# Optimization experiments

Measured on AMD Instinct MI355X. Metric: run time of the kernel, lower is better.

## Reference

```python
import jax, jax.numpy as jnp
import numpy as np

N_NODES = 50000
N_EDGES = 600000
D = 128
EPS = 1e-5
AVG_D_LOG = float(np.log(4 + 1))  # avg_d={'log': log(avg_d+1)}, avg_d=4


def setup_inputs() -> dict:
    key = jax.random.key(0)
    ks = jax.random.split(key, 8)
    h = jax.random.normal(ks[0], (N_NODES, D), dtype=jnp.float32)
    # guarantee every node has at least one incoming edge (self-loop)
    edge_dst = jnp.concatenate([
        jnp.arange(N_NODES, dtype=jnp.int64),
        jax.random.randint(ks[1], (N_EDGES - N_NODES,), 0, N_NODES).astype(jnp.int64),
    ])
    edge_src = jax.random.randint(ks[2], (N_EDGES,), 0, N_NODES).astype(jnp.int64)
    def lin(k, fan_in, fan_out):
        lim = 1.0 / np.sqrt(fan_in)
        return jax.random.uniform(k, (fan_in, fan_out), jnp.float32, -lim, lim)
    W_pre = lin(ks[3], 2 * D, D)
    b_pre = jnp.zeros((D,), jnp.float32)
    W_post = lin(ks[4], 12 * D + D, D)  # 4 aggregators * 3 scalers * D + in_dim
    b_post = jnp.zeros((D,), jnp.float32)
    W_mix = lin(ks[5], D, D)
    b_mix = jnp.zeros((D,), jnp.float32)
    return {"h": h, "edge_src": edge_src, "edge_dst": edge_dst,
            "W_pre": W_pre, "b_pre": b_pre, "W_post": W_post,
            "b_post": b_post, "W_mix": W_mix, "b_mix": b_mix}


def reference(h, edge_src, edge_dst, W_pre, b_pre, W_post, b_post, W_mix, b_mix):
    n = h.shape[0]
    # pretrans_edges: cat(src, dst) -> Linear -> ReLU (MLP act) -> ReLU (outer)
    z2 = jnp.concatenate([h[edge_src], h[edge_dst]], axis=1)        # [E, 2D]
    e = jax.nn.relu(z2 @ W_pre + b_pre)                             # [E, D]
    # multi-aggregator segment reduce over destination nodes
    deg = jax.ops.segment_sum(jnp.ones_like(edge_dst, jnp.float32), edge_dst, n)  # [N]
    inv_deg = 1.0 / deg[:, None]
    mean = jax.ops.segment_sum(e, edge_dst, n) * inv_deg
    mean_sq = jax.ops.segment_sum(e * e, edge_dst, n) * inv_deg
    std = jnp.sqrt(jax.nn.relu(mean_sq - mean * mean) + EPS)
    mx = jax.ops.segment_max(e, edge_dst, n)
    mn = jax.ops.segment_min(e, edge_dst, n)
    agg = jnp.concatenate([mean, mx, mn, std], axis=1)              # [N, 4D]
    # scalers: identity, amplification, attenuation
    log_d = jnp.log(deg + 1.0)[:, None]
    scaled = jnp.concatenate([agg, agg * (log_d / AVG_D_LOG), agg * (AVG_D_LOG / log_d)], axis=1)  # [N, 12D]
    # posttrans: cat(h, aggregated) -> Linear -> ReLU
    hp = jax.nn.relu(jnp.concatenate([h, scaled], axis=1) @ W_post + b_post)  # [N, D]
    # mixing network + residual (node_dim == out_dim)
    out = h + jax.nn.leaky_relu(hp @ W_mix + b_mix, negative_slope=0.01)
    return out
```

## Files before the change

### kernel.cpp

```cpp
#include <hip/hip_runtime.h>
#include <hip/hip_bf16.h>

#define N_NODES 50000
#define N_EDGES 600000
#define D 128
#define NB_SCAN 196

constexpr float AVG_D_LOG = 1.6094379124341003f;
constexpr float EPS_V = 1e-5f;

#define PQ_B     0ul
#define AGG_B    25600000ul
#define HBF_B    76800000ul
#define WPRET2_B 89600000ul
#define WPOSTT_B 89665536ul
#define WMIXT_B  90091520ul
#define DEGC_B   90124288ul
#define OFF_B    90324288ul
#define CUR_B    90524352ul
#define SRCS_B   90724352ul
#define BSUM_B   93124352ul

typedef __attribute__((ext_vector_type(8))) short bf16x8;
typedef __attribute__((ext_vector_type(4))) float f32x4;

__device__ __forceinline__ short f2b(float f) {
    unsigned u = __builtin_bit_cast(unsigned, f);
    u += 0x7fffu + ((u >> 16) & 1u);
    return (short)(u >> 16);
}
__device__ __forceinline__ unsigned pk2(float a, float b) {
    return (unsigned)(unsigned short)f2b(a) | ((unsigned)(unsigned short)f2b(b) << 16);
}
__device__ __forceinline__ float blo(unsigned u) { return __uint_as_float(u << 16); }
__device__ __forceinline__ float bhi(unsigned u) { return __uint_as_float(u & 0xffff0000u); }

__global__ __launch_bounds__(256) void prep_kernel(
    const float* __restrict__ h, const float* __restrict__ Wpre,
    const float* __restrict__ Wpost, const float* __restrict__ Wmix,
    short* __restrict__ hbf, short* __restrict__ wpreT2,
    short* __restrict__ wpostT, short* __restrict__ wmixT,
    int* __restrict__ degc, int* __restrict__ cursor)
{
    long i = (long)blockIdx.x * 256 + threadIdx.x;
    if (i < 6400000) { hbf[i] = f2b(h[i]); return; }
    i -= 6400000;
    if (i < 32768) {
        int n = i >> 7, k = i & 127;
        float v = (n < 128) ? Wpre[k * 128 + n] : Wpre[(k + 128) * 128 + (n - 128)];
        wpreT2[n * 128 + k] = f2b(v);
        return;
    }
    i -= 32768;
    if (i < 212992) { int k = i >> 7, n = i & 127; wpostT[n * 1664 + k] = f2b(Wpost[k * 128 + n]); return; }
    i -= 212992;
    if (i < 16384) { int k = i >> 7, n = i & 127; wmixT[n * 128 + k] = f2b(Wmix[k * 128 + n]); return; }
    i -= 16384;
    if (i < N_NODES) { degc[i] = 0; return; }
    i -= N_NODES;
    if (i < N_NODES) cursor[i] = 0;
}

__global__ __launch_bounds__(256) void hist_kernel(const int* __restrict__ edst, int* __restrict__ degc) {
    int e = blockIdx.x * 256 + threadIdx.x;
    if (e < N_EDGES) atomicAdd(&degc[edst[e]], 1);
}

__global__ __launch_bounds__(256) void scan1_kernel(const int* __restrict__ degc, int* __restrict__ bsum) {
    int n = blockIdx.x * 256 + threadIdx.x;
    int v = (n < N_NODES) ? degc[n] : 0;
#pragma unroll
    for (int o = 32; o > 0; o >>= 1) v += __shfl_down(v, o);
    __shared__ int w4[4];
    if ((threadIdx.x & 63) == 0) w4[threadIdx.x >> 6] = v;
    __syncthreads();
    if (threadIdx.x == 0) bsum[blockIdx.x] = w4[0] + w4[1] + w4[2] + w4[3];
}

__global__ void scan2_kernel(int* __restrict__ bsum, int* __restrict__ off) {
    if (threadIdx.x == 0 && blockIdx.x == 0) {
        int r = 0;
        for (int i = 0; i < NB_SCAN; i++) { int t = bsum[i]; bsum[i] = r; r += t; }
        off[N_NODES] = r;
    }
}

__global__ __launch_bounds__(256) void scan3_kernel(const int* __restrict__ degc,
                                                    const int* __restrict__ bsum, int* __restrict__ off) {
    __shared__ int sd[256];
    int tid = threadIdx.x;
    int n = blockIdx.x * 256 + tid;
    int v = (n < N_NODES) ? degc[n] : 0;
    sd[tid] = v;
    __syncthreads();
    for (int o = 1; o < 256; o <<= 1) {
        int t = (tid >= o) ? sd[tid - o] : 0;
        __syncthreads();
        sd[tid] += t;
        __syncthreads();
    }
    if (n < N_NODES) off[n] = sd[tid] - v + bsum[blockIdx.x];
}

__global__ __launch_bounds__(256) void scatter_kernel(const int* __restrict__ esrc, const int* __restrict__ edst,
                                                      const int* __restrict__ off, int* __restrict__ cursor,
                                                      int* __restrict__ srcs) {
    int e = blockIdx.x * 256 + threadIdx.x;
    if (e < N_EDGES) {
        int d = edst[e];
        int p = off[d] + atomicAdd(&cursor[d], 1);
        srcs[p] = esrc[e];
    }
}

__global__ __launch_bounds__(256) void gemm_pq_kernel(
    const short* __restrict__ hbf, const short* __restrict__ wpreT2,
    const float* __restrict__ bpre, short* __restrict__ PQ)
{
    __shared__ __align__(16) short As[128][72];
    __shared__ __align__(16) short Bs[256][72];

    const int tid = threadIdx.x;
    const int bn = blockIdx.x * 128;
    const int lane = tid & 63, wv = tid >> 6;
    const int lm = lane & 15, quad = lane >> 4;

    f32x4 acc[2][16];
#pragma unroll
    for (int a = 0; a < 2; a++)
#pragma unroll
        for (int b = 0; b < 16; b++) acc[a][b] = (f32x4){0.f, 0.f, 0.f, 0.f};

#pragma unroll
    for (int kc = 0; kc < 2; kc++) {
        __syncthreads();
#pragma unroll
        for (int t = 0; t < 4; t++) {
            int q = tid + t * 256;
            int m = q >> 3, seg = q & 7;
            int n = bn + m; if (n >= N_NODES) n = N_NODES - 1;
            *(int4*)&As[m][seg * 8] = *(const int4*)(hbf + (long)n * 128 + kc * 64 + seg * 8);
        }
#pragma unroll
        for (int t = 0; t < 8; t++) {
            int q = tid + t * 256;
            int n = q >> 3, seg = q & 7;
            *(int4*)&Bs[n][seg * 8] = *(const int4*)(wpreT2 + n * 128 + kc * 64 + seg * 8);
        }
        __syncthreads();
#pragma unroll
        for (int ks = 0; ks < 2; ks++) {
            const int ko = ks * 32 + quad * 8;
            bf16x8 a0 = *(const bf16x8*)&As[wv * 32 + lm][ko];
            bf16x8 a1 = *(const bf16x8*)&As[wv * 32 + 16 + lm][ko];
#pragma unroll
            for (int ct = 0; ct < 16; ct++) {
                bf16x8 b = *(const bf16x8*)&Bs[ct * 16 + lm][ko];
                acc[0][ct] = __builtin_amdgcn_mfma_f32_16x16x32_bf16(b, a0, acc[0][ct], 0, 0, 0);
                acc[1][ct] = __builtin_amdgcn_mfma_f32_16x16x32_bf16(b, a1, acc[1][ct], 0, 0, 0);
            }
        }
    }

#pragma unroll
    for (int rt = 0; rt < 2; rt++) {
        int row = wv * 32 + rt * 16 + lm;
        int n = bn + row;
        if (n >= N_NODES) continue;
        short* dst = PQ + (long)n * 256;
#pragma unroll
        for (int ct = 0; ct < 16; ct++) {
            int col = ct * 16 + quad * 4;
            float v0 = acc[rt][ct][0], v1 = acc[rt][ct][1], v2 = acc[rt][ct][2], v3 = acc[rt][ct][3];
            if (ct >= 8) {
                float4 bv = *(const float4*)(bpre + (col - 128));
                v0 += bv.x; v1 += bv.y; v2 += bv.z; v3 += bv.w;
            }
            int2 pkd; pkd.x = (int)pk2(v0, v1); pkd.y = (int)pk2(v2, v3);
            *(int2*)(dst + col) = pkd;
        }
    }
}

__global__ __launch_bounds__(256) void edgestats_kernel(
    const short* __restrict__ PQ, const int* __restrict__ srcs,
    const int* __restrict__ off, short* __restrict__ aggbf)
{
    const int wv = threadIdx.x >> 6, lane = threadIdx.x & 63;
    const int n = blockIdx.x * 4 + wv;
    const unsigned* Pb = (const unsigned*)PQ;

    const int s0 = __builtin_amdgcn_readfirstlane(off[n]);
    const int s1 = __builtin_amdgcn_readfirstlane(off[n + 1]);

    unsigned qu = Pb[(long)n * 128 + 64 + lane];
    const float qa = blo(qu), qb = bhi(qu);

    float sA = 0.f, sB = 0.f, qA = 0.f, qB = 0.f;
    float mxA = -1e30f, mxB = -1e30f, mnA = 1e30f, mnB = 1e30f;

    int p = s0;
    for (; p + 4 <= s1; p += 4) {
        int i0 = srcs[p], i1 = srcs[p + 1], i2 = srcs[p + 2], i3 = srcs[p + 3];
        unsigned u0 = Pb[(long)i0 * 128 + lane];
        unsigned u1 = Pb[(long)i1 * 128 + lane];
        unsigned u2 = Pb[(long)i2 * 128 + lane];
        unsigned u3 = Pb[(long)i3 * 128 + lane];
#pragma unroll
        for (int j = 0; j < 4; j++) {
            unsigned u = (j == 0) ? u0 : (j == 1) ? u1 : (j == 2) ? u2 : u3;
            float a = blo(u) + qa; a = a > 0.f ? a : 0.f;
            float b = bhi(u) + qb; b = b > 0.f ? b : 0.f;
            sA += a; sB += b; qA += a * a; qB += b * b;
            mxA = fmaxf(mxA, a); mxB = fmaxf(mxB, b);
            mnA = fminf(mnA, a); mnB = fminf(mnB, b);
        }
    }
    for (; p < s1; p++) {
        unsigned u = Pb[(long)srcs[p] * 128 + lane];
        float a = blo(u) + qa; a = a > 0.f ? a : 0.f;
        float b = bhi(u) + qb; b = b > 0.f ? b : 0.f;
        sA += a; sB += b; qA += a * a; qB += b * b;
        mxA = fmaxf(mxA, a); mxB = fmaxf(mxB, b);
        mnA = fminf(mnA, a); mnB = fminf(mnB, b);
    }

    float inv = 1.0f / (float)(s1 - s0);
    float mA = sA * inv, mB = sB * inv;
    float vA = qA * inv - mA * mA; vA = vA > 0.f ? vA : 0.f;
    float vB = qB * inv - mB * mB; vB = vB > 0.f ? vB : 0.f;
    float stA = sqrtf(vA + EPS_V), stB = sqrtf(vB + EPS_V);

    unsigned* ag = (unsigned*)(aggbf + (long)n * 512);
    ag[lane]       = pk2(mA, mB);
    ag[64 + lane]  = pk2(mxA, mxB);
    ag[128 + lane] = pk2(mnA, mnB);
    ag[192 + lane] = pk2(stA, stB);
}

__global__ __launch_bounds__(256) void node_kernel(
    const float* __restrict__ h, const short* __restrict__ hbf, const short* __restrict__ aggbf,
    const int* __restrict__ degc, const short* __restrict__ wpostT, const float* __restrict__ bpost,
    const short* __restrict__ wmixT, const float* __restrict__ bmix, float* __restrict__ out)
{
    __shared__ __align__(16) short As[128][72];
    __shared__ __align__(16) short Bs[128][72];
    __shared__ float sAmp[128], sAtt[128];

    const int tid = threadIdx.x;
    const int bn = blockIdx.x * 128;
    if (tid < 128) {
        int n = bn + tid; if (n >= N_NODES) n = N_NODES - 1;
        float d = (float)degc[n];
        float ld = logf(d + 1.0f);
        sAmp[tid] = ld * (1.0f / AVG_D_LOG);
        sAtt[tid] = AVG_D_LOG / ld;
    }
    __syncthreads();

    const int lane = tid & 63, wv = tid >> 6;
    const int lm = lane & 15, quad = lane >> 4;

    f32x4 acc[2][8];
#pragma unroll
    for (int a = 0; a < 2; a++)
#pragma unroll
        for (int b = 0; b < 8; b++) acc[a][b] = (f32x4){0.f, 0.f, 0.f, 0.f};

    for (int c = 0; c < 26; c++) {
        __syncthreads();
        const int r = c >> 1;
        const int half = (c & 1) * 64;
#pragma unroll
        for (int t = 0; t < 4; t++) {
            int q = tid + t * 256;
            int m = q >> 3, seg = q & 7;
            int n = bn + m; if (n >= N_NODES) n = N_NODES - 1;
            int4 v;
            if (r == 0) {
                v = *(const int4*)(hbf + (long)n * 128 + half + seg * 8);
            } else {
                int a = (r - 1) & 3, s = (r - 1) >> 2;
                v = *(const int4*)(aggbf + (long)n * 512 + a * 128 + half + seg * 8);
                if (s) {
                    float sc = (s == 1) ? sAmp[m] : sAtt[m];
                    unsigned* pu = (unsigned*)&v;
#pragma unroll
                    for (int j = 0; j < 4; j++) {
                        unsigned u = pu[j];
                        pu[j] = pk2(blo(u) * sc, bhi(u) * sc);
                    }
                }
            }
            *(int4*)&As[m][seg * 8] = v;
        }
#pragma unroll
        for (int t = 0; t < 4; t++) {
            int q = tid + t * 256;
            int n = q >> 3, seg = q & 7;
            *(int4*)&Bs[n][seg * 8] = *(const int4*)(wpostT + n * 1664 + c * 64 + seg * 8);
        }
        __syncthreads();
#pragma unroll
        for (int ks = 0; ks < 2; ks++) {
            const int ko = ks * 32 + quad * 8;
            bf16x8 a0 = *(const bf16x8*)&As[wv * 32 + lm][ko];
            bf16x8 a1 = *(const bf16x8*)&As[wv * 32 + 16 + lm][ko];
#pragma unroll
            for (int ct = 0; ct < 8; ct++) {
                bf16x8 b = *(const bf16x8*)&Bs[ct * 16 + lm][ko];
                acc[0][ct] = __builtin_amdgcn_mfma_f32_16x16x32_bf16(b, a0, acc[0][ct], 0, 0, 0);
                acc[1][ct] = __builtin_amdgcn_mfma_f32_16x16x32_bf16(b, a1, acc[1][ct], 0, 0, 0);
            }
        }
    }

#pragma unroll
    for (int rt = 0; rt < 2; rt++)
#pragma unroll
        for (int ct = 0; ct < 8; ct++) {
            float4 bv = *(const float4*)(bpost + ct * 16 + quad * 4);
            float v0 = acc[rt][ct][0] + bv.x; acc[rt][ct][0] = v0 > 0.f ? v0 : 0.f;
            float v1 = acc[rt][ct][1] + bv.y; acc[rt][ct][1] = v1 > 0.f ? v1 : 0.f;
            float v2 = acc[rt][ct][2] + bv.z; acc[rt][ct][2] = v2 > 0.f ? v2 : 0.f;
            float v3 = acc[rt][ct][3] + bv.w; acc[rt][ct][3] = v3 > 0.f ? v3 : 0.f;
        }

    f32x4 acc2[2][8];
#pragma unroll
    for (int a = 0; a < 2; a++)
#pragma unroll
        for (int b = 0; b < 8; b++) acc2[a][b] = (f32x4){0.f, 0.f, 0.f, 0.f};

#pragma unroll
    for (int kc = 0; kc < 2; kc++) {
        __syncthreads();
#pragma unroll
        for (int ctl = 0; ctl < 4; ctl++) {
            int ct = kc * 4 + ctl;
#pragma unroll
            for (int rt = 0; rt < 2; rt++) {
                int row = wv * 32 + rt * 16 + lm;
                int col = ctl * 16 + quad * 4;
                int2 pkd;
                pkd.x = (int)pk2(acc[rt][ct][0], acc[rt][ct][1]);
                pkd.y = (int)pk2(acc[rt][ct][2], acc[rt][ct][3]);
                *(int2*)&As[row][col] = pkd;
            }
        }
#pragma unroll
        for (int t = 0; t < 4; t++) {
            int q = tid + t * 256;
            int n = q >> 3, seg = q & 7;
            *(int4*)&Bs[n][seg * 8] = *(const int4*)(wmixT + n * 128 + kc * 64 + seg * 8);
        }
        __syncthreads();
#pragma unroll
        for (int ks = 0; ks < 2; ks++) {
            const int ko = ks * 32 + quad * 8;
            bf16x8 a0 = *(const bf16x8*)&As[wv * 32 + lm][ko];
            bf16x8 a1 = *(const bf16x8*)&As[wv * 32 + 16 + lm][ko];
#pragma unroll
            for (int ct = 0; ct < 8; ct++) {
                bf16x8 b = *(const bf16x8*)&Bs[ct * 16 + lm][ko];
                acc2[0][ct] = __builtin_amdgcn_mfma_f32_16x16x32_bf16(b, a0, acc2[0][ct], 0, 0, 0);
                acc2[1][ct] = __builtin_amdgcn_mfma_f32_16x16x32_bf16(b, a1, acc2[1][ct], 0, 0, 0);
            }
        }
    }

#pragma unroll
    for (int rt = 0; rt < 2; rt++) {
        int row = wv * 32 + rt * 16 + lm;
        int n = bn + row;
        if (n >= N_NODES) continue;
#pragma unroll
        for (int ct = 0; ct < 8; ct++) {
            int col = ct * 16 + quad * 4;
            float4 bv = *(const float4*)(bmix + col);
            float4 hv = *(const float4*)(h + (long)n * 128 + col);
            float4 o;
            float v0 = acc2[rt][ct][0] + bv.x; v0 = v0 > 0.f ? v0 : 0.01f * v0; o.x = hv.x + v0;
            float v1 = acc2[rt][ct][1] + bv.y; v1 = v1 > 0.f ? v1 : 0.01f * v1; o.y = hv.y + v1;
            float v2 = acc2[rt][ct][2] + bv.z; v2 = v2 > 0.f ? v2 : 0.01f * v2; o.z = hv.z + v2;
            float v3 = acc2[rt][ct][3] + bv.w; v3 = v3 > 0.f ? v3 : 0.01f * v3; o.w = hv.w + v3;
            *(float4*)(out + (long)n * 128 + col) = o;
        }
    }
}

extern "C" void kernel_launch(void* const* d_in, const int* in_sizes, int n_in,
                              void* d_out, int out_size, void* d_ws, size_t ws_size,
                              hipStream_t stream) {
    const float* h     = (const float*)d_in[0];
    const int*   esrc  = (const int*)d_in[1];
    const int*   edst  = (const int*)d_in[2];
    const float* Wpre  = (const float*)d_in[3];
    const float* bpre  = (const float*)d_in[4];
    const float* Wpost = (const float*)d_in[5];
    const float* bpost = (const float*)d_in[6];
    const float* Wmix  = (const float*)d_in[7];
    const float* bmix  = (const float*)d_in[8];
    float* out = (float*)d_out;
    char* ws = (char*)d_ws;

    short* PQ     = (short*)(ws + PQ_B);
    short* aggbf  = (short*)(ws + AGG_B);
    short* hbf    = (short*)(ws + HBF_B);
    short* wpreT2 = (short*)(ws + WPRET2_B);
    short* wpostT = (short*)(ws + WPOSTT_B);
    short* wmixT  = (short*)(ws + WMIXT_B);
    int*   degc   = (int*)(ws + DEGC_B);
    int*   off    = (int*)(ws + OFF_B);
    int*   cursor = (int*)(ws + CUR_B);
    int*   srcs   = (int*)(ws + SRCS_B);
    int*   bsum   = (int*)(ws + BSUM_B);

    prep_kernel<<<26415, 256, 0, stream>>>(h, Wpre, Wpost, Wmix, hbf, wpreT2, wpostT, wmixT, degc, cursor);
    hist_kernel<<<(N_EDGES + 255) / 256, 256, 0, stream>>>(edst, degc);
    scan1_kernel<<<NB_SCAN, 256, 0, stream>>>(degc, bsum);
    scan2_kernel<<<1, 64, 0, stream>>>(bsum, off);
    scan3_kernel<<<NB_SCAN, 256, 0, stream>>>(degc, bsum, off);
    scatter_kernel<<<(N_EDGES + 255) / 256, 256, 0, stream>>>(esrc, edst, off, cursor, srcs);
    gemm_pq_kernel<<<(N_NODES + 127) / 128, 256, 0, stream>>>(hbf, wpreT2, bpre, PQ);
    edgestats_kernel<<<N_NODES / 4, 256, 0, stream>>>(PQ, srcs, off, aggbf);
    node_kernel<<<(N_NODES + 127) / 128, 256, 0, stream>>>(h, hbf, aggbf, degc, wpostT, bpost, wmixT, bmix, out);
}
```

Measured before the change: 295.0 us.

## Factor degree scalers out of post GEMM into three accumulators; parallelize block scan

The node kernel no longer builds the amplified and attenuated aggregate copies in shared memory. The same aggregate tile is multiplied by three weight slices into separate accumulators, which are combined per row with amp and att scalars after the K loop. This drops the per-element bf16 rescaling and cuts K iterations from 26 to 10, with the node tile halved to 64 rows to fit the three accumulator sets. The single-thread block-sum scan is also replaced by a 256-thread shared-memory scan. The cost is a larger Bs tile, more registers per thread, and twice as many blocks, each reloading the full weight matrix.

```diff
diff --git a/kernel.cpp b/kernel.cpp
--- a/kernel.cpp
+++ b/kernel.cpp
@@ -77,12 +77,20 @@
     if (threadIdx.x == 0) bsum[blockIdx.x] = w4[0] + w4[1] + w4[2] + w4[3];
 }
 
-__global__ void scan2_kernel(int* __restrict__ bsum, int* __restrict__ off) {
-    if (threadIdx.x == 0 && blockIdx.x == 0) {
-        int r = 0;
-        for (int i = 0; i < NB_SCAN; i++) { int t = bsum[i]; bsum[i] = r; r += t; }
-        off[N_NODES] = r;
-    }
+__global__ __launch_bounds__(256) void scan2_kernel(int* __restrict__ bsum, int* __restrict__ off) {
+    __shared__ int sd[256];
+    int tid = threadIdx.x;
+    int v = (tid < NB_SCAN) ? bsum[tid] : 0;
+    sd[tid] = v;
+    __syncthreads();
+    for (int o = 1; o < 256; o <<= 1) {
+        int t = (tid >= o) ? sd[tid - o] : 0;
+        __syncthreads();
+        sd[tid] += t;
+        __syncthreads();
+    }
+    if (tid < NB_SCAN) bsum[tid] = sd[tid] - v;
+    if (tid == 0) off[N_NODES] = sd[255];
 }
 
 __global__ __launch_bounds__(256) void scan3_kernel(const int* __restrict__ degc,
@@ -243,56 +251,42 @@
     const int* __restrict__ degc, const short* __restrict__ wpostT, const float* __restrict__ bpost,
     const short* __restrict__ wmixT, const float* __restrict__ bmix, float* __restrict__ out)
 {
-    __shared__ __align__(16) short As[128][72];
-    __shared__ __align__(16) short Bs[128][72];
-    __shared__ float sAmp[128], sAtt[128];
+    __shared__ __align__(16) short As[64][72];
+    __shared__ __align__(16) short Bs[384][72];
+    __shared__ float sAmp[64], sAtt[64];
 
     const int tid = threadIdx.x;
-    const int bn = blockIdx.x * 128;
-    if (tid < 128) {
+    const int bn = blockIdx.x * 64;
+    if (tid < 64) {
         int n = bn + tid; if (n >= N_NODES) n = N_NODES - 1;
         float d = (float)degc[n];
         float ld = logf(d + 1.0f);
         sAmp[tid] = ld * (1.0f / AVG_D_LOG);
         sAtt[tid] = AVG_D_LOG / ld;
     }
-    __syncthreads();
 
     const int lane = tid & 63, wv = tid >> 6;
     const int lm = lane & 15, quad = lane >> 4;
-
-    f32x4 acc[2][8];
-#pragma unroll
-    for (int a = 0; a < 2; a++)
-#pragma unroll
-        for (int b = 0; b < 8; b++) acc[a][b] = (f32x4){0.f, 0.f, 0.f, 0.f};
-
-    for (int c = 0; c < 26; c++) {
-        __syncthreads();
-        const int r = c >> 1;
-        const int half = (c & 1) * 64;
-#pragma unroll
-        for (int t = 0; t < 4; t++) {
+    const int arow = wv * 16 + lm;
+
+    f32x4 Y1[8], Y2[8], Y3[8];
+#pragma unroll
+    for (int b = 0; b < 8; b++) {
+        Y1[b] = (f32x4){0.f, 0.f, 0.f, 0.f};
+        Y2[b] = (f32x4){0.f, 0.f, 0.f, 0.f};
+        Y3[b] = (f32x4){0.f, 0.f, 0.f, 0.f};
+    }
+
+    for (int c = 0; c < 10; c++) {
+        __syncthreads();
+#pragma unroll
+        for (int t = 0; t < 2; t++) {
             int q = tid + t * 256;
             int m = q >> 3, seg = q & 7;
             int n = bn + m; if (n >= N_NODES) n = N_NODES - 1;
-            int4 v;
-            if (r == 0) {
-                v = *(const int4*)(hbf + (long)n * 128 + half + seg * 8);
-            } else {
-                int a = (r - 1) & 3, s = (r - 1) >> 2;
-                v = *(const int4*)(aggbf + (long)n * 512 + a * 128 + half + seg * 8);
-                if (s) {
-                    float sc = (s == 1) ? sAmp[m] : sAtt[m];
-                    unsigned* pu = (unsigned*)&v;
-#pragma unroll
-                    for (int j = 0; j < 4; j++) {
-                        unsigned u = pu[j];
-                        pu[j] = pk2(blo(u) * sc, bhi(u) * sc);
-                    }
-                }
-            }
-            *(int4*)&As[m][seg * 8] = v;
+            const short* src = (c < 2) ? (hbf + (long)n * 128 + c * 64 + seg * 8)
+                                       : (aggbf + (long)n * 512 + (c - 2) * 64 + seg * 8);
+            *(int4*)&As[m][seg * 8] = *(const int4*)src;
         }
 #pragma unroll
         for (int t = 0; t < 4; t++) {
@@ -300,37 +294,65 @@
             int n = q >> 3, seg = q & 7;
             *(int4*)&Bs[n][seg * 8] = *(const int4*)(wpostT + n * 1664 + c * 64 + seg * 8);
         }
-        __syncthreads();
-#pragma unroll
-        for (int ks = 0; ks < 2; ks++) {
-            const int ko = ks * 32 + quad * 8;
-            bf16x8 a0 = *(const bf16x8*)&As[wv * 32 + lm][ko];
-            bf16x8 a1 = *(const bf16x8*)&As[wv * 32 + 16 + lm][ko];
-#pragma unroll
-            for (int ct = 0; ct < 8; ct++) {
-                bf16x8 b = *(const bf16x8*)&Bs[ct * 16 + lm][ko];
-                acc[0][ct] = __builtin_amdgcn_mfma_f32_16x16x32_bf16(b, a0, acc[0][ct], 0, 0, 0);
-                acc[1][ct] = __builtin_amdgcn_mfma_f32_16x16x32_bf16(b, a1, acc[1][ct], 0, 0, 0);
-            }
-        }
-    }
-
-#pragma unroll
-    for (int rt = 0; rt < 2; rt++)
+        if (c >= 2) {
+            const int k2 = 640 + (c - 2) * 64, k3 = 1152 + (c - 2) * 64;
+#pragma unroll
+            for (int t = 0; t < 4; t++) {
+                int q = tid + t * 256;
+                int n = q >> 3, seg = q & 7;
+                *(int4*)&Bs[128 + n][seg * 8] = *(const int4*)(wpostT + n * 1664 + k2 + seg * 8);
+                *(int4*)&Bs[256 + n][seg * 8] = *(const int4*)(wpostT + n * 1664 + k3 + seg * 8);
+            }
+        }
+        __syncthreads();
+        if (c >= 2) {
+#pragma unroll
+            for (int ks = 0; ks < 2; ks++) {
+                const int ko = ks * 32 + quad * 8;
+                bf16x8 a = *(const bf16x8*)&As[arow][ko];
+#pragma unroll
+                for (int ct = 0; ct < 8; ct++) {
+                    bf16x8 b1 = *(const bf16x8*)&Bs[ct * 16 + lm][ko];
+                    bf16x8 b2 = *(const bf16x8*)&Bs[128 + ct * 16 + lm][ko];
+                    bf16x8 b3 = *(const bf16x8*)&Bs[256 + ct * 16 + lm][ko];
+                    Y1[ct] = __builtin_amdgcn_mfma_f32_16x16x32_bf16(b1, a, Y1[ct], 0, 0, 0);
+                    Y2[ct] = __builtin_amdgcn_mfma_f32_16x16x32_bf16(b2, a, Y2[ct], 0, 0, 0);
+                    Y3[ct] = __builtin_amdgcn_mfma_f32_16x16x32_bf16(b3, a, Y3[ct], 0, 0, 0);
+                }
+            }
+        } else {
+#pragma unroll
+            for (int ks = 0; ks < 2; ks++) {
+                const int ko = ks * 32 + quad * 8;
+                bf16x8 a = *(const bf16x8*)&As[arow][ko];
+#pragma unroll
+                for (int ct = 0; ct < 8; ct++) {
+                    bf16x8 b1 = *(const bf16x8*)&Bs[ct * 16 + lm][ko];
+                    Y1[ct] = __builtin_amdgcn_mfma_f32_16x16x32_bf16(b1, a, Y1[ct], 0, 0, 0);
+                }
+            }
+        }
+    }
+
+    {
+        const float amp = sAmp[arow], att = sAtt[arow];
 #pragma unroll
         for (int ct = 0; ct < 8; ct++) {
             float4 bv = *(const float4*)(bpost + ct * 16 + quad * 4);
-            float v0 = acc[rt][ct][0] + bv.x; acc[rt][ct][0] = v0 > 0.f ? v0 : 0.f;
-            float v1 = acc[rt][ct][1] + bv.y; acc[rt][ct][1] = v1 > 0.f ? v1 : 0.f;
-            float v2 = acc[rt][ct][2] + bv.z; acc[rt][ct][2] = v2 > 0.f ? v2 : 0.f;
-            float v3 = acc[rt][ct][3] + bv.w; acc[rt][ct][3] = v3 > 0.f ? v3 : 0.f;
-        }
-
-    f32x4 acc2[2][8];
-#pragma unroll
-    for (int a = 0; a < 2; a++)
-#pragma unroll
-        for (int b = 0; b < 8; b++) acc2[a][b] = (f32x4){0.f, 0.f, 0.f, 0.f};
+            float v0 = Y1[ct][0] + amp * Y2[ct][0] + att * Y3[ct][0] + bv.x;
+            float v1 = Y1[ct][1] + amp * Y2[ct][1] + att * Y3[ct][1] + bv.y;
+            float v2 = Y1[ct][2] + amp * Y2[ct][2] + att * Y3[ct][2] + bv.z;
+            float v3 = Y1[ct][3] + amp * Y2[ct][3] + att * Y3[ct][3] + bv.w;
+            Y1[ct][0] = v0 > 0.f ? v0 : 0.f;
+            Y1[ct][1] = v1 > 0.f ? v1 : 0.f;
+            Y1[ct][2] = v2 > 0.f ? v2 : 0.f;
+            Y1[ct][3] = v3 > 0.f ? v3 : 0.f;
+        }
+    }
+
+    f32x4 acc2[8];
+#pragma unroll
+    for (int b = 0; b < 8; b++) acc2[b] = (f32x4){0.f, 0.f, 0.f, 0.f};
 
 #pragma unroll
     for (int kc = 0; kc < 2; kc++) {
@@ -338,15 +360,11 @@
 #pragma unroll
         for (int ctl = 0; ctl < 4; ctl++) {
             int ct = kc * 4 + ctl;
-#pragma unroll
-            for (int rt = 0; rt < 2; rt++) {
-                int row = wv * 32 + rt * 16 + lm;
-                int col = ctl * 16 + quad * 4;
-                int2 pkd;
-                pkd.x = (int)pk2(acc[rt][ct][0], acc[rt][ct][1]);
-                pkd.y = (int)pk2(acc[rt][ct][2], acc[rt][ct][3]);
-                *(int2*)&As[row][col] = pkd;
-            }
+            int col = ctl * 16 + quad * 4;
+            int2 pkd;
+            pkd.x = (int)pk2(Y1[ct][0], Y1[ct][1]);
+            pkd.y = (int)pk2(Y1[ct][2], Y1[ct][3]);
+            *(int2*)&As[arow][col] = pkd;
         }
 #pragma unroll
         for (int t = 0; t < 4; t++) {
@@ -358,33 +376,30 @@
 #pragma unroll
         for (int ks = 0; ks < 2; ks++) {
             const int ko = ks * 32 + quad * 8;
-            bf16x8 a0 = *(const bf16x8*)&As[wv * 32 + lm][ko];
-            bf16x8 a1 = *(const bf16x8*)&As[wv * 32 + 16 + lm][ko];
+            bf16x8 a = *(const bf16x8*)&As[arow][ko];
 #pragma unroll
             for (int ct = 0; ct < 8; ct++) {
                 bf16x8 b = *(const bf16x8*)&Bs[ct * 16 + lm][ko];
-                acc2[0][ct] = __builtin_amdgcn_mfma_f32_16x16x32_bf16(b, a0, acc2[0][ct], 0, 0, 0);
-                acc2[1][ct] = __builtin_amdgcn_mfma_f32_16x16x32_bf16(b, a1, acc2[1][ct], 0, 0, 0);
-            }
-        }
-    }
-
-#pragma unroll
-    for (int rt = 0; rt < 2; rt++) {
-        int row = wv * 32 + rt * 16 + lm;
-        int n = bn + row;
-        if (n >= N_NODES) continue;
-#pragma unroll
-        for (int ct = 0; ct < 8; ct++) {
-            int col = ct * 16 + quad * 4;
-            float4 bv = *(const float4*)(bmix + col);
-            float4 hv = *(const float4*)(h + (long)n * 128 + col);
-            float4 o;
-            float v0 = acc2[rt][ct][0] + bv.x; v0 = v0 > 0.f ? v0 : 0.01f * v0; o.x = hv.x + v0;
-            float v1 = acc2[rt][ct][1] + bv.y; v1 = v1 > 0.f ? v1 : 0.01f * v1; o.y = hv.y + v1;
-            float v2 = acc2[rt][ct][2] + bv.z; v2 = v2 > 0.f ? v2 : 0.01f * v2; o.z = hv.z + v2;
-            float v3 = acc2[rt][ct][3] + bv.w; v3 = v3 > 0.f ? v3 : 0.01f * v3; o.w = hv.w + v3;
-            *(float4*)(out + (long)n * 128 + col) = o;
+                acc2[ct] = __builtin_amdgcn_mfma_f32_16x16x32_bf16(b, a, acc2[ct], 0, 0, 0);
+            }
+        }
+    }
+
+    {
+        int n = bn + arow;
+        if (n < N_NODES) {
+#pragma unroll
+            for (int ct = 0; ct < 8; ct++) {
+                int col = ct * 16 + quad * 4;
+                float4 bv = *(const float4*)(bmix + col);
+                float4 hv = *(const float4*)(h + (long)n * 128 + col);
+                float4 o;
+                float v0 = acc2[ct][0] + bv.x; v0 = v0 > 0.f ? v0 : 0.01f * v0; o.x = hv.x + v0;
+                float v1 = acc2[ct][1] + bv.y; v1 = v1 > 0.f ? v1 : 0.01f * v1; o.y = hv.y + v1;
+                float v2 = acc2[ct][2] + bv.z; v2 = v2 > 0.f ? v2 : 0.01f * v2; o.z = hv.z + v2;
+                float v3 = acc2[ct][3] + bv.w; v3 = v3 > 0.f ? v3 : 0.01f * v3; o.w = hv.w + v3;
+                *(float4*)(out + (long)n * 128 + col) = o;
+            }
         }
     }
 }
@@ -419,10 +434,10 @@
     prep_kernel<<<26415, 256, 0, stream>>>(h, Wpre, Wpost, Wmix, hbf, wpreT2, wpostT, wmixT, degc, cursor);
     hist_kernel<<<(N_EDGES + 255) / 256, 256, 0, stream>>>(edst, degc);
     scan1_kernel<<<NB_SCAN, 256, 0, stream>>>(degc, bsum);
-    scan2_kernel<<<1, 64, 0, stream>>>(bsum, off);
+    scan2_kernel<<<1, 256, 0, stream>>>(bsum, off);
     scan3_kernel<<<NB_SCAN, 256, 0, stream>>>(degc, bsum, off);
     scatter_kernel<<<(N_EDGES + 255) / 256, 256, 0, stream>>>(esrc, edst, off, cursor, srcs);
     gemm_pq_kernel<<<(N_NODES + 127) / 128, 256, 0, stream>>>(hbf, wpreT2, bpre, PQ);
     edgestats_kernel<<<N_NODES / 4, 256, 0, stream>>>(PQ, srcs, off, aggbf);
-    node_kernel<<<(N_NODES + 127) / 128, 256, 0, stream>>>(h, hbf, aggbf, degc, wpostT, bpost, wmixT, bmix, out);
-}
+    node_kernel<<<(N_NODES + 63) / 64, 256, 0, stream>>>(h, hbf, aggbf, degc, wpostT, bpost, wmixT, bmix, out);
+}
```

Result: slower. 388.5 us (+31.7%).

## Prefetch next GEMM tile into registers, parallelize block scan, widen edge gather unroll

Applied to the files above, without the earlier changes.

The node GEMM now loads the next K-chunk of activations and weights into registers while MFMAs run on the current LDS tile, so global-load latency overlaps with compute. The single-threaded block-sum scan becomes a 256-thread shared-memory scan. The edge statistics loop unrolls to 8 gathers in flight instead of 4. These add register pressure, which may lower occupancy.

```diff
diff --git a/kernel.cpp b/kernel.cpp
--- a/kernel.cpp
+++ b/kernel.cpp
@@ -77,12 +77,20 @@
     if (threadIdx.x == 0) bsum[blockIdx.x] = w4[0] + w4[1] + w4[2] + w4[3];
 }
 
-__global__ void scan2_kernel(int* __restrict__ bsum, int* __restrict__ off) {
-    if (threadIdx.x == 0 && blockIdx.x == 0) {
-        int r = 0;
-        for (int i = 0; i < NB_SCAN; i++) { int t = bsum[i]; bsum[i] = r; r += t; }
-        off[N_NODES] = r;
-    }
+__global__ __launch_bounds__(256) void scan2_kernel(int* __restrict__ bsum, int* __restrict__ off) {
+    __shared__ int sd[256];
+    int tid = threadIdx.x;
+    int v = (tid < NB_SCAN) ? bsum[tid] : 0;
+    sd[tid] = v;
+    __syncthreads();
+    for (int o = 1; o < 256; o <<= 1) {
+        int t = (tid >= o) ? sd[tid - o] : 0;
+        __syncthreads();
+        sd[tid] += t;
+        __syncthreads();
+    }
+    if (tid < NB_SCAN) bsum[tid] = sd[tid] - v;
+    if (tid == 0) off[N_NODES] = sd[255];
 }
 
 __global__ __launch_bounds__(256) void scan3_kernel(const int* __restrict__ degc,
@@ -200,17 +208,14 @@
     float mxA = -1e30f, mxB = -1e30f, mnA = 1e30f, mnB = 1e30f;
 
     int p = s0;
-    for (; p + 4 <= s1; p += 4) {
-        int i0 = srcs[p], i1 = srcs[p + 1], i2 = srcs[p + 2], i3 = srcs[p + 3];
-        unsigned u0 = Pb[(long)i0 * 128 + lane];
-        unsigned u1 = Pb[(long)i1 * 128 + lane];
-        unsigned u2 = Pb[(long)i2 * 128 + lane];
-        unsigned u3 = Pb[(long)i3 * 128 + lane];
-#pragma unroll
-        for (int j = 0; j < 4; j++) {
-            unsigned u = (j == 0) ? u0 : (j == 1) ? u1 : (j == 2) ? u2 : u3;
-            float a = blo(u) + qa; a = a > 0.f ? a : 0.f;
-            float b = bhi(u) + qb; b = b > 0.f ? b : 0.f;
+    for (; p + 8 <= s1; p += 8) {
+        unsigned u[8];
+#pragma unroll
+        for (int j = 0; j < 8; j++) u[j] = Pb[(long)srcs[p + j] * 128 + lane];
+#pragma unroll
+        for (int j = 0; j < 8; j++) {
+            float a = blo(u[j]) + qa; a = a > 0.f ? a : 0.f;
+            float b = bhi(u[j]) + qb; b = b > 0.f ? b : 0.f;
             sA += a; sB += b; qA += a * a; qB += b * b;
             mxA = fmaxf(mxA, a); mxB = fmaxf(mxB, b);
             mnA = fminf(mnA, a); mnB = fminf(mnB, b);
@@ -267,40 +272,54 @@
 #pragma unroll
         for (int b = 0; b < 8; b++) acc[a][b] = (f32x4){0.f, 0.f, 0.f, 0.f};
 
+    int4 rA[4], rB[4];
+#pragma unroll
+    for (int t = 0; t < 4; t++) {
+        int q = tid + t * 256;
+        int m = q >> 3, seg = q & 7;
+        int n = bn + m; if (n >= N_NODES) n = N_NODES - 1;
+        rA[t] = *(const int4*)(hbf + (long)n * 128 + seg * 8);
+        rB[t] = *(const int4*)(wpostT + m * 1664 + seg * 8);
+    }
+
     for (int c = 0; c < 26; c++) {
         __syncthreads();
         const int r = c >> 1;
-        const int half = (c & 1) * 64;
+        const int s = (r == 0) ? 0 : ((r - 1) >> 2);
 #pragma unroll
         for (int t = 0; t < 4; t++) {
             int q = tid + t * 256;
             int m = q >> 3, seg = q & 7;
-            int n = bn + m; if (n >= N_NODES) n = N_NODES - 1;
-            int4 v;
-            if (r == 0) {
-                v = *(const int4*)(hbf + (long)n * 128 + half + seg * 8);
-            } else {
-                int a = (r - 1) & 3, s = (r - 1) >> 2;
-                v = *(const int4*)(aggbf + (long)n * 512 + a * 128 + half + seg * 8);
-                if (s) {
-                    float sc = (s == 1) ? sAmp[m] : sAtt[m];
-                    unsigned* pu = (unsigned*)&v;
-#pragma unroll
-                    for (int j = 0; j < 4; j++) {
-                        unsigned u = pu[j];
-                        pu[j] = pk2(blo(u) * sc, bhi(u) * sc);
-                    }
+            int4 v = rA[t];
+            if (s) {
+                float sc = (s == 1) ? sAmp[m] : sAtt[m];
+                unsigned* pu = (unsigned*)&v;
+#pragma unroll
+                for (int j = 0; j < 4; j++) {
+                    unsigned u = pu[j];
+                    pu[j] = pk2(blo(u) * sc, bhi(u) * sc);
                 }
             }
             *(int4*)&As[m][seg * 8] = v;
-        }
-#pragma unroll
-        for (int t = 0; t < 4; t++) {
-            int q = tid + t * 256;
-            int n = q >> 3, seg = q & 7;
-            *(int4*)&Bs[n][seg * 8] = *(const int4*)(wpostT + n * 1664 + c * 64 + seg * 8);
-        }
-        __syncthreads();
+            *(int4*)&Bs[m][seg * 8] = rB[t];
+        }
+        __syncthreads();
+        if (c < 25) {
+            const int c1 = c + 1;
+            const int r1 = c1 >> 1;
+            const int half1 = (c1 & 1) * 64;
+#pragma unroll
+            for (int t = 0; t < 4; t++) {
+                int q = tid + t * 256;
+                int m = q >> 3, seg = q & 7;
+                int n = bn + m; if (n >= N_NODES) n = N_NODES - 1;
+                const short* srcA = (r1 == 0)
+                    ? (hbf + (long)n * 128 + half1 + seg * 8)
+                    : (aggbf + (long)n * 512 + ((r1 - 1) & 3) * 128 + half1 + seg * 8);
+                rA[t] = *(const int4*)srcA;
+                rB[t] = *(const int4*)(wpostT + m * 1664 + c1 * 64 + seg * 8);
+            }
+        }
 #pragma unroll
         for (int ks = 0; ks < 2; ks++) {
             const int ko = ks * 32 + quad * 8;
@@ -419,7 +438,7 @@
     prep_kernel<<<26415, 256, 0, stream>>>(h, Wpre, Wpost, Wmix, hbf, wpreT2, wpostT, wmixT, degc, cursor);
     hist_kernel<<<(N_EDGES + 255) / 256, 256, 0, stream>>>(edst, degc);
     scan1_kernel<<<NB_SCAN, 256, 0, stream>>>(degc, bsum);
-    scan2_kernel<<<1, 64, 0, stream>>>(bsum, off);
+    scan2_kernel<<<1, 256, 0, stream>>>(bsum, off);
     scan3_kernel<<<NB_SCAN, 256, 0, stream>>>(degc, bsum, off);
     scatter_kernel<<<(N_EDGES + 255) / 256, 256, 0, stream>>>(esrc, edst, off, cursor, srcs);
     gemm_pq_kernel<<<(N_NODES + 127) / 128, 256, 0, stream>>>(hbf, wpreT2, bpre, PQ);
```

After: 310.8 us. +5.4%, slower.
